# Kernel optimization log

Hardware: AMD Instinct MI355X
Metric: run time of the kernel (lower is better)

## Reference

```python
import jax, jax.numpy as jnp
import numpy as np

N = 100000  # nodes
E = 1600000  # edges
D_IN = 64
D_H = 64


def _sage_conv(x, src, dst, w_l, b_l, w_r):
    """PyG SAGEConv (mean aggr): lin_l(mean_j x_j) + lin_r(x_i).
    w_l, w_r: [out, in]; b_l: [out]."""
    # scatter-mean of source features onto target nodes
    msg_sum = jax.ops.segment_sum(x[src], dst, num_segments=N)  # [N, in]
    cnt = jax.ops.segment_sum(jnp.ones((src.shape[0],), x.dtype), dst, num_segments=N)
    mean = msg_sum / jnp.maximum(cnt, 1.0)[:, None]
    return mean @ w_l.T + b_l + x @ w_r.T


def setup_inputs() -> dict:
    key = jax.random.key(0)
    ks = jax.random.split(key, 8)
    x = jax.random.normal(ks[0], (N, D_IN), dtype=jnp.float32)
    edge_index = jax.random.randint(ks[1], (2, E), 0, N, dtype=jnp.int64)
    s = 1.0 / np.sqrt(D_IN)
    w_l1 = jax.random.uniform(ks[2], (D_H, D_IN), jnp.float32, -s, s)
    b_l1 = jnp.zeros((D_H,), jnp.float32)
    w_r1 = jax.random.uniform(ks[3], (D_H, D_IN), jnp.float32, -s, s)
    s2 = 1.0 / np.sqrt(D_H)
    w_l2 = jax.random.uniform(ks[4], (D_H, D_H), jnp.float32, -s2, s2)
    b_l2 = jnp.zeros((D_H,), jnp.float32)
    w_r2 = jax.random.uniform(ks[5], (D_H, D_H), jnp.float32, -s2, s2)
    return {"x": x, "edge_index": edge_index,
            "w_l1": w_l1, "b_l1": b_l1, "w_r1": w_r1,
            "w_l2": w_l2, "b_l2": b_l2, "w_r2": w_r2}


def reference(x, edge_index, w_l1, b_l1, w_r1, w_l2, b_l2, w_r2):
    src, dst = edge_index[0], edge_index[1]
    h = jax.nn.relu(_sage_conv(x, src, dst, w_l1, b_l1, w_r1))
    out = _sage_conv(h, src, dst, w_l2, b_l2, w_r2)
    return out
```

## Files before the change

kernel.cpp:

```cpp
#include <hip/hip_runtime.h>

#define N_NODES 100000
#define N_EDGES 1600000
#define D 64

#define BSHIFT 7
#define BNODES (1 << BSHIFT)
#define NB ((N_NODES + BNODES - 1) / BNODES)
#define NPAD (NB * BNODES)
#define PB 256
#define TILE ((N_EDGES + PB - 1) / PB)
#define CAP 2432
#define MAXB 4096
#define CAST_BLKS 512
#define QBLKS ((N_NODES * D / 4 + 1023) / 1024)
#define HPARTS (N_NODES / 16)

typedef __attribute__((ext_vector_type(8))) short short8;
typedef __attribute__((ext_vector_type(4))) float float4v;
typedef __attribute__((ext_vector_type(2))) unsigned uint2v;
typedef __attribute__((ext_vector_type(4))) unsigned uint4v;

__device__ __forceinline__ unsigned short f2bf(float f) {
    unsigned u = __float_as_uint(f);
    u = (u + 0x7fffu + ((u >> 16) & 1u)) >> 16;
    return (unsigned short)u;
}
__device__ __forceinline__ unsigned cvtpk(float a, float b) {
    unsigned r;
    asm("v_cvt_pk_bf16_f32 %0, %1, %2" : "=v"(r) : "v"(a), "v"(b));
    return r;
}

__device__ __forceinline__ float4 bf16x4_to_f4(uint2 v) {
    float4 r;
    r.x = __uint_as_float(v.x << 16);
    r.y = __uint_as_float(v.x & 0xffff0000u);
    r.z = __uint_as_float(v.y << 16);
    r.w = __uint_as_float(v.y & 0xffff0000u);
    return r;
}

__global__ __launch_bounds__(1024) void front(const float* __restrict__ x,
                                              unsigned short* __restrict__ xb,
                                              float* __restrict__ partial,
                                              const int* __restrict__ src,
                                              const int* __restrict__ dst,
                                              int* __restrict__ gcnt,
                                              int* __restrict__ part) {
    __shared__ float red[16];
    __shared__ int hist[NB];
    __shared__ int lcur[NB];
    __shared__ int gbase[NB];
    __shared__ int ebuf[TILE];
    __shared__ int gtgt[TILE];

    int tid = threadIdx.x;

    if (blockIdx.x < CAST_BLKS) {
        float m = 0.0f;
        int stride = CAST_BLKS * 1024;
        for (int i = blockIdx.x * 1024 + tid; i < N_NODES * D / 4; i += stride) {
            float4 v = ((const float4*)x)[i];
            ushort4 o;
            o.x = f2bf(v.x); o.y = f2bf(v.y); o.z = f2bf(v.z); o.w = f2bf(v.w);
            ((ushort4*)xb)[i] = o;
            m = fmaxf(m, fmaxf(fmaxf(fabsf(v.x), fabsf(v.y)), fmaxf(fabsf(v.z), fabsf(v.w))));
        }
        for (int off = 32; off >= 1; off >>= 1) m = fmaxf(m, __shfl_xor(m, off, 64));
        if ((tid & 63) == 0) red[tid >> 6] = m;
        __syncthreads();
        if (tid == 0) {
            float mm = 0.0f;
#pragma unroll
            for (int w = 0; w < 16; ++w) mm = fmaxf(mm, red[w]);
            partial[blockIdx.x] = mm;
        }
        return;
    }

    int bid = blockIdx.x - CAST_BLKS;
    for (int i = tid; i < NB; i += 1024) hist[i] = 0;
    __syncthreads();

    int lo = bid * TILE;

    unsigned pk[7];
    int bk[7];
#pragma unroll
    for (int k = 0; k < 7; ++k) {
        int e = lo + tid + k * 1024;
        if (tid + k * 1024 < TILE) {
            int dd = dst[e];
            int ss = src[e];
            int b = dd >> BSHIFT;
            pk[k] = ((unsigned)ss << BSHIFT) | (unsigned)(dd & (BNODES - 1));
            bk[k] = b;
            atomicAdd(&hist[b], 1);
        } else {
            bk[k] = -1;
        }
    }
    __syncthreads();

    int h = (tid < NB) ? hist[tid] : 0;
    if (tid < NB)
        gbase[tid] = tid * CAP + (h ? atomicAdd(&gcnt[tid], h) : 0);
    int val = h;
    gtgt[tid] = val;
    __syncthreads();
    for (int off = 1; off < 1024; off <<= 1) {
        int u = (tid >= off) ? gtgt[tid - off] : 0;
        __syncthreads();
        val += u;
        gtgt[tid] = val;
        __syncthreads();
    }
    if (tid < NB) {
        hist[tid] = val - h;
        lcur[tid] = val - h;
    }
    __syncthreads();

#pragma unroll
    for (int k = 0; k < 7; ++k) {
        if (bk[k] >= 0) {
            int b = bk[k];
            int p = atomicAdd(&lcur[b], 1);
            ebuf[p] = (int)pk[k];
            gtgt[p] = gbase[b] + (p - hist[b]);
        }
    }
    __syncthreads();

    for (int i = tid; i < TILE; i += 1024)
        part[gtgt[i]] = ebuf[i];
}

__device__ __forceinline__ void quant_body(int i, const unsigned short* __restrict__ inb,
                                           unsigned char* __restrict__ out8, float s) {
    uint2 v = ((const uint2*)inb)[i];
    float4 f = bf16x4_to_f4(v);
    int q0 = min(127, max(-127, __float2int_rn(f.x * s))) + 128;
    int q1 = min(127, max(-127, __float2int_rn(f.y * s))) + 128;
    int q2 = min(127, max(-127, __float2int_rn(f.z * s))) + 128;
    int q3 = min(127, max(-127, __float2int_rn(f.w * s))) + 128;
    ((unsigned*)out8)[i] = (unsigned)q0 | ((unsigned)q1 << 8) |
                           ((unsigned)q2 << 16) | ((unsigned)q3 << 24);
}

__device__ __forceinline__ float fold_partials(const float* __restrict__ partial,
                                               int n, float* red, float* bc) {
    int tid = threadIdx.x;
    float m = 0.0f;
    for (int i = tid; i < n; i += 1024) m = fmaxf(m, partial[i]);
    for (int off = 32; off >= 1; off >>= 1) m = fmaxf(m, __shfl_xor(m, off, 64));
    if ((tid & 63) == 0) red[tid >> 6] = m;
    __syncthreads();
    if (tid == 0) {
        float mm = 0.0f;
#pragma unroll
        for (int w = 0; w < 16; ++w) mm = fmaxf(mm, red[w]);
        *bc = mm;
    }
    __syncthreads();
    return *bc;
}

__global__ __launch_bounds__(1024) void back(const int* __restrict__ gcnt,
                                             const int* __restrict__ part,
                                             int* __restrict__ rbeg,
                                             int* __restrict__ rend,
                                             int* __restrict__ sorted_src,
                                             const unsigned short* __restrict__ xb,
                                             unsigned char* __restrict__ x8,
                                             const float* __restrict__ partial,
                                             unsigned* __restrict__ amax_store,
                                             const float* __restrict__ wl1,
                                             const float* __restrict__ wr1,
                                             unsigned short* __restrict__ wb1,
                                             const float* __restrict__ wl2,
                                             const float* __restrict__ wr2,
                                             unsigned short* __restrict__ wb2) {
    __shared__ int in_buf[MAXB];
    __shared__ int out_buf[MAXB];
    __shared__ int hist[BNODES];
    __shared__ int exs[BNODES];
    __shared__ int cursor[BNODES];
    __shared__ float red[16];
    __shared__ float bc;

    int tid = threadIdx.x;

    if (blockIdx.x >= NB + QBLKS) {
        int i = (blockIdx.x - NB - QBLKS) * 1024 + tid;
        int j = i & 8191;
        int o = j >> 7, kk = j & 127;
        if (i < 8192) {
            float v = (kk < D) ? wl1[o * D + kk] : wr1[o * D + (kk - D)];
            wb1[j] = f2bf(v);
        } else {
            float v = (kk < D) ? wl2[o * D + kk] : wr2[o * D + (kk - D)];
            wb2[j] = f2bf(v);
        }
        return;
    }

    if (blockIdx.x >= NB) {
        float A = fold_partials(partial, CAST_BLKS, red, &bc);
        if (blockIdx.x == NB && tid == 0) *amax_store = __float_as_uint(A);
        float s = (A > 0.0f) ? 127.0f / A : 0.0f;
        int i = (blockIdx.x - NB) * 1024 + tid;
        if (i < N_NODES * D / 4) quant_body(i, xb, x8, s);
        return;
    }

    int k = blockIdx.x;
    int base  = k * CAP;
    int count = gcnt[k];

    for (int i = tid; i < BNODES; i += 1024) hist[i] = 0;
    __syncthreads();

    for (int i = tid; i < count; i += 1024) {
        int w = part[base + i];
        in_buf[i] = w;
        atomicAdd(&hist[w & (BNODES - 1)], 1);
    }
    __syncthreads();
    if (tid < 64) {
        int a = hist[2 * tid], b = hist[2 * tid + 1];
        int s = a + b, incl = s;
        for (int off = 1; off < 64; off <<= 1) {
            int t = __shfl_up(incl, off, 64);
            if (tid >= off) incl += t;
        }
        int excl = incl - s;
        exs[2 * tid] = excl;
        exs[2 * tid + 1] = excl + a;
    }
    __syncthreads();
    if (tid < BNODES) {
        int node = k * BNODES + tid;
        if (node < N_NODES) {
            rbeg[node] = base + exs[tid];
            rend[node] = base + exs[tid] + hist[tid];
        }
        cursor[tid] = exs[tid];
    }
    __syncthreads();
    for (int i = tid; i < count; i += 1024) {
        int w = in_buf[i];
        int r = atomicAdd(&cursor[w & (BNODES - 1)], 1);
        out_buf[r] = w >> BSHIFT;
    }
    __syncthreads();
    for (int i = tid; i < count; i += 1024)
        sorted_src[base + i] = out_buf[i];
}

__global__ __launch_bounds__(1024) void quant8f(const unsigned short* __restrict__ inb,
                                                unsigned char* __restrict__ out8,
                                                const float* __restrict__ partial,
                                                unsigned* __restrict__ amax_store) {
    __shared__ float red[16];
    __shared__ float bc;
    float A = fold_partials(partial, HPARTS, red, &bc);
    if (blockIdx.x == 0 && threadIdx.x == 0) *amax_store = __float_as_uint(A);
    float s = (A > 0.0f) ? 127.0f / A : 0.0f;
    int i = blockIdx.x * 1024 + threadIdx.x;
    if (i < N_NODES * D / 4) quant_body(i, inb, out8, s);
}

#define ACCW(w, kk) { aLo[kk] += (w) & 0x00FF00FFu; \
                      aHi[kk] += __builtin_amdgcn_perm(0u, (w), 0x04030401u); }
#define ACC4(v) { ACCW((v).x, 0) ACCW((v).y, 1) ACCW((v).z, 2) ACCW((v).w, 3) }

__global__ __launch_bounds__(512, 8) void sage8(
    const int* __restrict__ rbeg, const int* __restrict__ rend,
    const int* __restrict__ nbr,
    const unsigned char* __restrict__ tab8,
    const unsigned short* __restrict__ selfb,
    const unsigned* __restrict__ amax_bits,
    const unsigned short* __restrict__ wb,
    const float* __restrict__ b_l,
    float* __restrict__ out,
    unsigned short* __restrict__ outb,
    float* __restrict__ hpart,
    int apply_relu)
{
    __shared__ unsigned short a_s[16][136];
    __shared__ float st[16][68];
    __shared__ float bias[D];
    __shared__ float wred[4];

    int tid = threadIdx.x;
    if (tid < D) bias[tid] = b_l[tid];

    int wave = tid >> 6;
    int lane = tid & 63;
    int nsel = lane >> 5;
    int l32  = lane & 31;
    int g    = l32 >> 2;
    int c    = l32 & 3;
    int arow = wave * 2 + nsel;
    int node = blockIdx.x * 16 + arow;

    float A  = __uint_as_float(*amax_bits);
    float gs = A * (1.0f / 127.0f);

    int begin = rbeg[node];
    int end   = rend[node];

    uint2v xv = {0, 0};
    if (l32 < 16)
        xv = __builtin_nontemporal_load((const uint2v*)&selfb[(size_t)node * D + 4 * l32]);

    unsigned c16 = (unsigned)(c << 4);
    unsigned aLo[4] = {0, 0, 0, 0};
    unsigned aHi[4] = {0, 0, 0, 0};
    for (int base = begin; base < end; base += 32) {
        int m = end - base;
        bool a0 = (g < m), a1 = (8 + g < m), a2 = (16 + g < m), a3 = (24 + g < m);
        int s0 = 0, s1 = 0, s2 = 0, s3 = 0;
        if (a0) s0 = nbr[base + g];
        if (a1) s1 = nbr[base + 8 + g];
        if (a2) s2 = nbr[base + 16 + g];
        if (a3) s3 = nbr[base + 24 + g];
        uint4 v0, v1, v2, v3;
        if (a0) v0 = *(const uint4*)(tab8 + ((((unsigned)s0) << 6) | c16));
        if (a1) v1 = *(const uint4*)(tab8 + ((((unsigned)s1) << 6) | c16));
        if (a2) v2 = *(const uint4*)(tab8 + ((((unsigned)s2) << 6) | c16));
        if (a3) v3 = *(const uint4*)(tab8 + ((((unsigned)s3) << 6) | c16));
        if (a0) { ACC4(v0) }
        if (a1) { ACC4(v1) }
        if (a2) { ACC4(v2) }
        if (a3) { ACC4(v3) }
    }

#pragma unroll
    for (int off = 4; off <= 16; off <<= 1) {
#pragma unroll
        for (int k = 0; k < 4; ++k) {
            aLo[k] += (unsigned)__shfl_xor((int)aLo[k], off, 64);
            aHi[k] += (unsigned)__shfl_xor((int)aHi[k], off, 64);
        }
    }

    int   deg  = end - begin;
    float invd = 1.0f / fmaxf((float)deg, 1.0f);
    float sc   = gs * invd;
    float nofs = -128.0f * (float)deg * sc;

    {
        unsigned lo01 = (g & 2) ? aLo[1] : aLo[0];
        unsigned lo23 = (g & 2) ? aLo[3] : aLo[2];
        unsigned wLo  = (g & 4) ? lo23 : lo01;
        unsigned hi01 = (g & 2) ? aHi[1] : aHi[0];
        unsigned hi23 = (g & 2) ? aHi[3] : aHi[2];
        unsigned wHi  = (g & 4) ? hi23 : hi01;
        int sh = (g & 1) << 4;
        float d0 = (float)((wLo >> sh) & 0xFFFFu);
        float d1 = (float)((wHi >> sh) & 0xFFFFu);
        float f0 = fmaf(d0, sc, nofs);
        float f1 = fmaf(d1, sc, nofs);
        *(unsigned*)&a_s[arow][16 * c + 2 * g] = cvtpk(f0, f1);
    }
    if (l32 < 16)
        *(uint2v*)&a_s[arow][64 + 4 * l32] = xv;
    __syncthreads();

    if (wave < 4) {
        int quad = lane >> 4;
        int cc   = lane & 15;

        float4v acc = {0.f, 0.f, 0.f, 0.f};
#pragma unroll
        for (int kk = 0; kk < 4; ++kk) {
            short8 af = *(const short8*)&a_s[cc][kk * 32 + quad * 8];
            short8 bf = *(const short8*)(wb + (size_t)(wave * 16 + cc) * 128 + kk * 32 + quad * 8);
            acc = __builtin_amdgcn_mfma_f32_16x16x32_bf16(af, bf, acc, 0, 0, 0);
        }

        int o = wave * 16 + cc;
        float bv = bias[o];
        float vv[4];
#pragma unroll
        for (int r = 0; r < 4; ++r) {
            float v = acc[r] + bv;
            if (apply_relu) v = fmaxf(v, 0.0f);
            vv[r] = v;
            st[quad * 4 + r][o] = v;
        }
        if (hpart) {
            float m = fmaxf(fmaxf(fabsf(vv[0]), fabsf(vv[1])),
                            fmaxf(fabsf(vv[2]), fabsf(vv[3])));
            for (int off = 32; off >= 1; off >>= 1) m = fmaxf(m, __shfl_xor(m, off, 64));
            if (lane == 0) wred[wave] = m;
        }
    }
    __syncthreads();

    if (wave >= 4) {
        int idx = tid - 256;
        if (outb) {
            if (idx < 128) {
                int row = idx >> 3, c8 = idx & 7;
                const float* p = &st[row][c8 * 8];
                float4v f0 = *(const float4v*)p;
                float4v f1 = *(const float4v*)(p + 4);
                uint4v q;
                q[0] = cvtpk(f0[0], f0[1]); q[1] = cvtpk(f0[2], f0[3]);
                q[2] = cvtpk(f1[0], f1[1]); q[3] = cvtpk(f1[2], f1[3]);
                __builtin_nontemporal_store(q,
                    (uint4v*)&outb[((size_t)(blockIdx.x * 16 + row)) * D + 8 * c8]);
            }
        } else {
            int row = idx >> 4, c4 = idx & 15;
            uint4v q = *(const uint4v*)&st[row][c4 * 4];
            __builtin_nontemporal_store(q,
                (uint4v*)&out[((size_t)(blockIdx.x * 16 + row)) * D + 4 * c4]);
        }
        if (hpart && idx == 0)
            hpart[blockIdx.x] = fmaxf(fmaxf(wred[0], wred[1]), fmaxf(wred[2], wred[3]));
    }
}

extern "C" void kernel_launch(void* const* d_in, const int* in_sizes, int n_in,
                              void* d_out, int out_size, void* d_ws, size_t ws_size,
                              hipStream_t stream) {
    const float* x    = (const float*)d_in[0];
    const int*   ei   = (const int*)d_in[1];
    const float* w_l1 = (const float*)d_in[2];
    const float* b_l1 = (const float*)d_in[3];
    const float* w_r1 = (const float*)d_in[4];
    const float* w_l2 = (const float*)d_in[5];
    const float* b_l2 = (const float*)d_in[6];
    const float* w_r2 = (const float*)d_in[7];
    float* out = (float*)d_out;

    const int* src = ei;
    const int* dst = ei + N_EDGES;

    unsigned* scales   = (unsigned*)d_ws;
    int* gcnt          = (int*)d_ws + 4;
    int* rbeg          = gcnt + NB;
    int* rend          = rbeg + NPAD;
    int* part          = rend + NPAD;
    int* sorted_src    = part + NB * CAP;
    unsigned short* xb = (unsigned short*)(sorted_src + NB * CAP);
    unsigned short* hb = xb + (size_t)N_NODES * D;
    unsigned char* x8  = (unsigned char*)(hb + (size_t)N_NODES * D);
    unsigned char* h8  = x8 + (size_t)N_NODES * D;
    unsigned short* wb1 = (unsigned short*)(h8 + (size_t)N_NODES * D);
    unsigned short* wb2 = wb1 + D * 2 * D;
    float* partA       = (float*)(wb2 + D * 2 * D);

    (void)hipMemsetAsync(d_ws, 0, 16 + NB * sizeof(int), stream);

    front<<<dim3(CAST_BLKS + PB), dim3(1024), 0, stream>>>(x, xb, partA,
                                                           src, dst, gcnt, part);
    back<<<dim3(NB + QBLKS + 16), dim3(1024), 0, stream>>>(gcnt, part,
                                                           rbeg, rend, sorted_src,
                                                           xb, x8, partA, &scales[0],
                                                           w_l1, w_r1, wb1,
                                                           w_l2, w_r2, wb2);

    dim3 lblk(512);
    dim3 lgrid(N_NODES / 16);
    sage8<<<lgrid, lblk, 0, stream>>>(rbeg, rend, sorted_src, x8, xb,
                                      &scales[0], wb1, b_l1,
                                      (float*)nullptr, hb, partA, 1);
    quant8f<<<dim3(QBLKS), dim3(1024), 0, stream>>>(hb, h8, partA, &scales[1]);
    sage8<<<lgrid, lblk, 0, stream>>>(rbeg, rend, sorted_src, h8, hb,
                                      &scales[1], wb2, b_l2,
                                      out, (unsigned short*)nullptr,
                                      (float*)nullptr, 0);
}
```

Before: 220.3 us.

## Make sage8 persistent and prefetch next tile's row bounds and neighbor ids

The sage8 launch goes from one block per 16-node tile to a fixed grid of 1024 blocks that loop over tiles with a grid-stride loop. While the current tile is being processed, each block loads the next tile's row offsets and its first 32 neighbor indices. Neighbor indices are now read with one coalesced load per lane and handed out with shuffles, instead of a separate scalar load per group. This aims to hide index-fetch latency and cut per-block launch and setup cost. In exchange, the smaller grid may lower occupancy and load balance across uneven node degrees.

```diff
diff --git a/kernel.cpp b/kernel.cpp
--- a/kernel.cpp
+++ b/kernel.cpp
@@ -14,7 +14,9 @@
 #define MAXB 4096
 #define CAST_BLKS 512
 #define QBLKS ((N_NODES * D / 4 + 1023) / 1024)
-#define HPARTS (N_NODES / 16)
+#define NT (N_NODES / 16)
+#define SGRID 1024
+#define HPARTS NT
 
 typedef __attribute__((ext_vector_type(8))) short short8;
 typedef __attribute__((ext_vector_type(4))) float float4v;
@@ -304,125 +306,145 @@
     int g    = l32 >> 2;
     int c    = l32 & 3;
     int arow = wave * 2 + nsel;
-    int node = blockIdx.x * 16 + arow;
 
     float A  = __uint_as_float(*amax_bits);
     float gs = A * (1.0f / 127.0f);
-
-    int begin = rbeg[node];
-    int end   = rend[node];
-
-    uint2v xv = {0, 0};
-    if (l32 < 16)
-        xv = __builtin_nontemporal_load((const uint2v*)&selfb[(size_t)node * D + 4 * l32]);
-
     unsigned c16 = (unsigned)(c << 4);
-    unsigned aLo[4] = {0, 0, 0, 0};
-    unsigned aHi[4] = {0, 0, 0, 0};
-    for (int base = begin; base < end; base += 32) {
-        int m = end - base;
-        bool a0 = (g < m), a1 = (8 + g < m), a2 = (16 + g < m), a3 = (24 + g < m);
-        int s0 = 0, s1 = 0, s2 = 0, s3 = 0;
-        if (a0) s0 = nbr[base + g];
-        if (a1) s1 = nbr[base + 8 + g];
-        if (a2) s2 = nbr[base + 16 + g];
-        if (a3) s3 = nbr[base + 24 + g];
-        uint4 v0, v1, v2, v3;
-        if (a0) v0 = *(const uint4*)(tab8 + ((((unsigned)s0) << 6) | c16));
-        if (a1) v1 = *(const uint4*)(tab8 + ((((unsigned)s1) << 6) | c16));
-        if (a2) v2 = *(const uint4*)(tab8 + ((((unsigned)s2) << 6) | c16));
-        if (a3) v3 = *(const uint4*)(tab8 + ((((unsigned)s3) << 6) | c16));
-        if (a0) { ACC4(v0) }
-        if (a1) { ACC4(v1) }
-        if (a2) { ACC4(v2) }
-        if (a3) { ACC4(v3) }
-    }
-
-#pragma unroll
-    for (int off = 4; off <= 16; off <<= 1) {
-#pragma unroll
-        for (int k = 0; k < 4; ++k) {
-            aLo[k] += (unsigned)__shfl_xor((int)aLo[k], off, 64);
-            aHi[k] += (unsigned)__shfl_xor((int)aHi[k], off, 64);
-        }
-    }
-
-    int   deg  = end - begin;
-    float invd = 1.0f / fmaxf((float)deg, 1.0f);
-    float sc   = gs * invd;
-    float nofs = -128.0f * (float)deg * sc;
-
-    {
-        unsigned lo01 = (g & 2) ? aLo[1] : aLo[0];
-        unsigned lo23 = (g & 2) ? aLo[3] : aLo[2];
-        unsigned wLo  = (g & 4) ? lo23 : lo01;
-        unsigned hi01 = (g & 2) ? aHi[1] : aHi[0];
-        unsigned hi23 = (g & 2) ? aHi[3] : aHi[2];
-        unsigned wHi  = (g & 4) ? hi23 : hi01;
-        int sh = (g & 1) << 4;
-        float d0 = (float)((wLo >> sh) & 0xFFFFu);
-        float d1 = (float)((wHi >> sh) & 0xFFFFu);
-        float f0 = fmaf(d0, sc, nofs);
-        float f1 = fmaf(d1, sc, nofs);
-        *(unsigned*)&a_s[arow][16 * c + 2 * g] = cvtpk(f0, f1);
-    }
-    if (l32 < 16)
-        *(uint2v*)&a_s[arow][64 + 4 * l32] = xv;
-    __syncthreads();
-
-    if (wave < 4) {
-        int quad = lane >> 4;
-        int cc   = lane & 15;
-
-        float4v acc = {0.f, 0.f, 0.f, 0.f};
-#pragma unroll
-        for (int kk = 0; kk < 4; ++kk) {
-            short8 af = *(const short8*)&a_s[cc][kk * 32 + quad * 8];
-            short8 bf = *(const short8*)(wb + (size_t)(wave * 16 + cc) * 128 + kk * 32 + quad * 8);
-            acc = __builtin_amdgcn_mfma_f32_16x16x32_bf16(af, bf, acc, 0, 0, 0);
-        }
-
-        int o = wave * 16 + cc;
-        float bv = bias[o];
-        float vv[4];
-#pragma unroll
-        for (int r = 0; r < 4; ++r) {
-            float v = acc[r] + bv;
-            if (apply_relu) v = fmaxf(v, 0.0f);
-            vv[r] = v;
-            st[quad * 4 + r][o] = v;
-        }
-        if (hpart) {
-            float m = fmaxf(fmaxf(fabsf(vv[0]), fabsf(vv[1])),
-                            fmaxf(fabsf(vv[2]), fabsf(vv[3])));
-            for (int off = 32; off >= 1; off >>= 1) m = fmaxf(m, __shfl_xor(m, off, 64));
-            if (lane == 0) wred[wave] = m;
-        }
-    }
-    __syncthreads();
-
-    if (wave >= 4) {
-        int idx = tid - 256;
-        if (outb) {
-            if (idx < 128) {
-                int row = idx >> 3, c8 = idx & 7;
-                const float* p = &st[row][c8 * 8];
-                float4v f0 = *(const float4v*)p;
-                float4v f1 = *(const float4v*)(p + 4);
-                uint4v q;
-                q[0] = cvtpk(f0[0], f0[1]); q[1] = cvtpk(f0[2], f0[3]);
-                q[2] = cvtpk(f1[0], f1[1]); q[3] = cvtpk(f1[2], f1[3]);
+
+    int tile = blockIdx.x;
+    int begin = rbeg[tile * 16 + arow];
+    int end   = rend[tile * 16 + arow];
+    int id0   = (begin + l32 < end) ? __builtin_nontemporal_load(&nbr[begin + l32]) : 0;
+
+    for (; tile < NT; tile += SGRID) {
+        int node = tile * 16 + arow;
+        int nt2  = tile + SGRID;
+
+        int b2 = 0, e2 = 0;
+        if (nt2 < NT) {
+            b2 = rbeg[nt2 * 16 + arow];
+            e2 = rend[nt2 * 16 + arow];
+        }
+
+        uint2v xv = {0, 0};
+        if (l32 < 16)
+            xv = __builtin_nontemporal_load((const uint2v*)&selfb[(size_t)node * D + 4 * l32]);
+
+        unsigned aLo[4] = {0, 0, 0, 0};
+        unsigned aHi[4] = {0, 0, 0, 0};
+        int idc = id0;
+        for (int base = begin; base < end; base += 32) {
+            int m = end - base; if (m > 32) m = 32;
+            if (base != begin)
+                idc = (l32 < m) ? __builtin_nontemporal_load(&nbr[base + l32]) : 0;
+            int s0 = __shfl(idc, nsel * 32 + g,      64);
+            int s1 = __shfl(idc, nsel * 32 + 8 + g,  64);
+            int s2 = __shfl(idc, nsel * 32 + 16 + g, 64);
+            int s3 = __shfl(idc, nsel * 32 + 24 + g, 64);
+            bool a0 = (g < m), a1 = (8 + g < m), a2 = (16 + g < m), a3 = (24 + g < m);
+            uint4 v0, v1, v2, v3;
+            if (a0) v0 = *(const uint4*)(tab8 + ((((unsigned)s0) << 6) | c16));
+            if (a1) v1 = *(const uint4*)(tab8 + ((((unsigned)s1) << 6) | c16));
+            if (a2) v2 = *(const uint4*)(tab8 + ((((unsigned)s2) << 6) | c16));
+            if (a3) v3 = *(const uint4*)(tab8 + ((((unsigned)s3) << 6) | c16));
+            if (a0) { ACC4(v0) }
+            if (a1) { ACC4(v1) }
+            if (a2) { ACC4(v2) }
+            if (a3) { ACC4(v3) }
+        }
+
+#pragma unroll
+        for (int off = 4; off <= 16; off <<= 1) {
+#pragma unroll
+            for (int k = 0; k < 4; ++k) {
+                aLo[k] += (unsigned)__shfl_xor((int)aLo[k], off, 64);
+                aHi[k] += (unsigned)__shfl_xor((int)aHi[k], off, 64);
+            }
+        }
+
+        int id2 = 0;
+        if (nt2 < NT && b2 + l32 < e2)
+            id2 = __builtin_nontemporal_load(&nbr[b2 + l32]);
+
+        int   deg  = end - begin;
+        float invd = 1.0f / fmaxf((float)deg, 1.0f);
+        float sc   = gs * invd;
+        float nofs = -128.0f * (float)deg * sc;
+
+        {
+            unsigned lo01 = (g & 2) ? aLo[1] : aLo[0];
+            unsigned lo23 = (g & 2) ? aLo[3] : aLo[2];
+            unsigned wLo  = (g & 4) ? lo23 : lo01;
+            unsigned hi01 = (g & 2) ? aHi[1] : aHi[0];
+            unsigned hi23 = (g & 2) ? aHi[3] : aHi[2];
+            unsigned wHi  = (g & 4) ? hi23 : hi01;
+            int sh = (g & 1) << 4;
+            float d0 = (float)((wLo >> sh) & 0xFFFFu);
+            float d1 = (float)((wHi >> sh) & 0xFFFFu);
+            float f0 = fmaf(d0, sc, nofs);
+            float f1 = fmaf(d1, sc, nofs);
+            *(unsigned*)&a_s[arow][16 * c + 2 * g] = cvtpk(f0, f1);
+        }
+        if (l32 < 16)
+            *(uint2v*)&a_s[arow][64 + 4 * l32] = xv;
+        __syncthreads();
+
+        if (wave < 4) {
+            int quad = lane >> 4;
+            int cc   = lane & 15;
+
+            float4v acc = {0.f, 0.f, 0.f, 0.f};
+#pragma unroll
+            for (int kk = 0; kk < 4; ++kk) {
+                short8 af = *(const short8*)&a_s[cc][kk * 32 + quad * 8];
+                short8 bf = *(const short8*)(wb + (size_t)(wave * 16 + cc) * 128 + kk * 32 + quad * 8);
+                acc = __builtin_amdgcn_mfma_f32_16x16x32_bf16(af, bf, acc, 0, 0, 0);
+            }
+
+            int o = wave * 16 + cc;
+            float bv = bias[o];
+            float vv[4];
+#pragma unroll
+            for (int r = 0; r < 4; ++r) {
+                float v = acc[r] + bv;
+                if (apply_relu) v = fmaxf(v, 0.0f);
+                vv[r] = v;
+                st[quad * 4 + r][o] = v;
+            }
+            if (hpart) {
+                float m = fmaxf(fmaxf(fabsf(vv[0]), fabsf(vv[1])),
+                                fmaxf(fabsf(vv[2]), fabsf(vv[3])));
+                for (int off = 32; off >= 1; off >>= 1) m = fmaxf(m, __shfl_xor(m, off, 64));
+                if (lane == 0) wred[wave] = m;
+            }
+        }
+        __syncthreads();
+
+        if (wave >= 4) {
+            int idx = tid - 256;
+            if (outb) {
+                if (idx < 128) {
+                    int row = idx >> 3, c8 = idx & 7;
+                    const float* p = &st[row][c8 * 8];
+                    float4v f0 = *(const float4v*)p;
+                    float4v f1 = *(const float4v*)(p + 4);
+                    uint4v q;
+                    q[0] = cvtpk(f0[0], f0[1]); q[1] = cvtpk(f0[2], f0[3]);
+                    q[2] = cvtpk(f1[0], f1[1]); q[3] = cvtpk(f1[2], f1[3]);
+                    __builtin_nontemporal_store(q,
+                        (uint4v*)&outb[((size_t)(tile * 16 + row)) * D + 8 * c8]);
+                }
+            } else {
+                int row = idx >> 4, c4 = idx & 15;
+                uint4v q = *(const uint4v*)&st[row][c4 * 4];
                 __builtin_nontemporal_store(q,
-                    (uint4v*)&outb[((size_t)(blockIdx.x * 16 + row)) * D + 8 * c8]);
+                    (uint4v*)&out[((size_t)(tile * 16 + row)) * D + 4 * c4]);
             }
-        } else {
-            int row = idx >> 4, c4 = idx & 15;
-            uint4v q = *(const uint4v*)&st[row][c4 * 4];
-            __builtin_nontemporal_store(q,
-                (uint4v*)&out[((size_t)(blockIdx.x * 16 + row)) * D + 4 * c4]);
-        }
-        if (hpart && idx == 0)
-            hpart[blockIdx.x] = fmaxf(fmaxf(wred[0], wred[1]), fmaxf(wred[2], wred[3]));
+            if (hpart && idx == 0)
+                hpart[tile] = fmaxf(fmaxf(wred[0], wred[1]), fmaxf(wred[2], wred[3]));
+        }
+
+        begin = b2; end = e2; id0 = id2;
     }
 }
 
@@ -467,7 +489,7 @@
                                                            w_l2, w_r2, wb2);
 
     dim3 lblk(512);
-    dim3 lgrid(N_NODES / 16);
+    dim3 lgrid(SGRID);
     sage8<<<lgrid, lblk, 0, stream>>>(rbeg, rend, sorted_src, x8, xb,
                                       &scales[0], wb1, b_l1,
                                       (float*)nullptr, hb, partA, 1);
```

Result: slower. 259.5 us (+17.8%).
